# Optimization experiments

Hardware: AMD Instinct MI355X
Metric: run time of the kernel (lower is better)

The kernel has to match this reference:

```python
import math
import jax, jax.numpy as jnp
import numpy as np

B, S, H, BOT, RD, N, K = 4, 2048, 1024, 128, 48, 4096, 8

def setup_inputs() -> dict:
    key = jax.random.key(0)
    ks = jax.random.split(key, 12)
    hidden_states = jax.random.normal(ks[0], (B, S, H), jnp.float32)
    q_proj_w = jax.random.normal(ks[1], (BOT, H), jnp.float32) * (1.0 / math.sqrt(H))
    router_w = jax.random.normal(ks[2], (RD, BOT), jnp.float32) * (1.0 / math.sqrt(BOT))
    aux_keys = jax.random.normal(ks[3], (N, BOT), jnp.float32) * 0.01
    aux_values = jax.random.normal(ks[4], (N, H), jnp.float32) * 0.02
    # reliability per slot (log-domain additive mask derived from lifecycle state)
    reliability_mask = jax.random.uniform(ks[5], (N,), jnp.float32)
    unc_w1 = jax.random.normal(ks[6], (H // 4, H), jnp.float32) * (1.0 / math.sqrt(H))
    unc_b1 = jnp.zeros((H // 4,), jnp.float32)
    unc_w2 = jax.random.normal(ks[7], (1, H // 4), jnp.float32) * 0.02
    unc_b2 = jnp.zeros((1,), jnp.float32)
    gate_w1 = jnp.asarray(0.5, jnp.float32)
    gate_bias = jnp.asarray(-1.0, jnp.float32)
    return {"hidden_states": hidden_states, "q_proj_w": q_proj_w, "router_w": router_w,
            "aux_keys": aux_keys, "aux_values": aux_values, "reliability_mask": reliability_mask,
            "unc_w1": unc_w1, "unc_b1": unc_b1, "unc_w2": unc_w2, "unc_b2": unc_b2,
            "gate_w1": gate_w1, "gate_bias": gate_bias}

def reference(hidden_states, q_proj_w, router_w, aux_keys, aux_values, reliability_mask,
              unc_w1, unc_b1, unc_w2, unc_b2, gate_w1, gate_bias):
    # --- SlotRouter: project query/keys to router_dim, score, mask, top-k ---
    query = jnp.einsum('bsh,dh->bsd', hidden_states, q_proj_w)        # [B,S,BOT]
    rq = jnp.einsum('bsd,rd->bsr', query, router_w)                   # [B,S,RD]
    rk = jnp.einsum('nd,rd->nr', aux_keys, router_w)                  # [N,RD]
    scores = jnp.einsum('bsr,nr->bsn', rq, rk) / math.sqrt(RD)        # [B,S,N]
    scores = scores + reliability_mask[None, None, :]
    top_scores, top_idx = jax.lax.top_k(scores, K)                    # [B,S,K]
    # --- UncertaintyEstimator (HIDDEN_VARIANCE) ---
    mean = hidden_states.mean(axis=-1, keepdims=True)
    variance = ((hidden_states - mean) ** 2).mean(axis=-1)            # [B,S]
    log_var = jnp.log1p(variance)
    normalized_var = log_var / (log_var.mean() + 1e-6)
    h1 = jax.nn.gelu(jnp.einsum('bsh,fh->bsf', hidden_states, unc_w1) + unc_b1, approximate=False)
    learned = (jnp.einsum('bsf,of->bso', h1, unc_w2) + unc_b2)[..., 0]
    uncertainty = jnp.clip(normalized_var * 0.5 + jax.nn.sigmoid(learned) * 2.5, 0.0, 5.0)
    # --- Gate-1 scalar gate + slot aggregation ---
    gate = jax.nn.sigmoid(gate_w1 * uncertainty + gate_bias)          # [B,S]
    w = jax.nn.softmax(top_scores, axis=-1)                           # [B,S,K]
    v = aux_values[top_idx]                                           # [B,S,K,H]
    agg = jnp.einsum('bsk,bskh->bsh', w, v)
    out = hidden_states + gate[..., None] * agg
    return out
```

## Files before the change

### kernel.cpp

```cpp
#include <hip/hip_runtime.h>
#include <hip/hip_bf16.h>
#include <math.h>
#include <stdint.h>

#define NT 256
constexpr int Hc = 1024, BOTc = 128, RDc = 48, Nc = 4096;
constexpr int ROWS = 8192;
constexpr float INV_SQRT_RD = 0.14433756729740643f;

typedef short bf16x8 __attribute__((ext_vector_type(8)));
typedef float f32x4 __attribute__((ext_vector_type(4)));

__device__ __forceinline__ uint32_t umin32(uint32_t a, uint32_t b) { return a < b ? a : b; }
__device__ __forceinline__ uint32_t umax32(uint32_t a, uint32_t b) { return a > b ? a : b; }
__device__ __forceinline__ void ce_asc(uint32_t& x, uint32_t& y) {
  uint32_t lo = umin32(x, y), hi = umax32(x, y); x = lo; y = hi;
}
__device__ __forceinline__ uint32_t pack_score(float s, int slot) {
  uint32_t u = __float_as_uint(s);
  u = (u & 0x80000000u) ? ~u : (u | 0x80000000u);
  return (u & 0xFFFFF000u) | (uint32_t)slot;
}
__device__ __forceinline__ float unpack_score(uint32_t p) {
  uint32_t m = p & 0xFFFFF000u;
  uint32_t f = (m & 0x80000000u) ? (m ^ 0x80000000u) : ~m;
  return __uint_as_float(f);
}
__device__ __forceinline__ void merge_top8(uint32_t a[8], const uint32_t b[8]) {
  uint32_t m[8];
#pragma unroll
  for (int i = 0; i < 8; ++i) m[i] = umax32(a[i], b[7 - i]);
  ce_asc(m[0], m[4]); ce_asc(m[1], m[5]); ce_asc(m[2], m[6]); ce_asc(m[3], m[7]);
  ce_asc(m[0], m[2]); ce_asc(m[1], m[3]); ce_asc(m[4], m[6]); ce_asc(m[5], m[7]);
  ce_asc(m[0], m[1]); ce_asc(m[2], m[3]); ce_asc(m[4], m[5]); ce_asc(m[6], m[7]);
#pragma unroll
  for (int i = 0; i < 8; ++i) a[i] = m[i];
}
__device__ __forceinline__ void top8_insert(uint32_t top[8], uint32_t p) {
  if (p > top[0]) {
    top[0] = p;
    ce_asc(top[0], top[1]); ce_asc(top[1], top[2]); ce_asc(top[2], top[3]);
    ce_asc(top[3], top[4]); ce_asc(top[4], top[5]); ce_asc(top[5], top[6]);
    ce_asc(top[6], top[7]);
  }
}
__device__ __forceinline__ uint16_t bf16bits(float x) {
  uint32_t u = __float_as_uint(x);
  return (uint16_t)(((u + 0x7FFFu + ((u >> 16) & 1u)) >> 16) & 0xFFFFu);
}
__device__ __forceinline__ float bf2f(uint16_t h) {
  return __uint_as_float((uint32_t)h << 16);
}

constexpr int GP_W48 = 64, GP_RK = 768, GP_HB = 1024, GP_CVW = 32, GP_CVA = 512;
__global__ __launch_bounds__(256) void k_prep_all(
    const float* __restrict__ hidden, const float* __restrict__ q_proj_w,
    const float* __restrict__ router_w, const float* __restrict__ aux_keys,
    const float* __restrict__ aux_values, const float* __restrict__ rel,
    const float* __restrict__ unc_w1,
    uint16_t* __restrict__ xb, float* __restrict__ log_var,
    uint16_t* __restrict__ wcat, uint16_t* __restrict__ avb,
    uint16_t* __restrict__ rk_b) {
  int bid = blockIdx.x;
  int tid = threadIdx.x;
  if (bid < GP_W48) {
    __shared__ float rw[BOTc];
    int j = bid;
    if (j >= RDc) {
      for (int hh = tid; hh < Hc; hh += NT) wcat[(size_t)(256 + j) * Hc + hh] = 0;
      return;
    }
    for (int d = tid; d < BOTc; d += NT) rw[d] = router_w[j * BOTc + d];
    __syncthreads();
    float acc[4] = {0.f, 0.f, 0.f, 0.f};
#pragma unroll 4
    for (int d = 0; d < BOTc; ++d) {
      float r = rw[d];
#pragma unroll
      for (int jj = 0; jj < 4; ++jj)
        acc[jj] = fmaf(r, q_proj_w[d * Hc + tid + 256 * jj], acc[jj]);
    }
#pragma unroll
    for (int jj = 0; jj < 4; ++jj)
      wcat[(size_t)(256 + j) * Hc + tid + 256 * jj] = bf16bits(acc[jj]);
    return;
  }
  bid -= GP_W48;
  if (bid < GP_RK) {
    int gid = bid * NT + tid;
    int n = gid / RDc, r = gid - n * RDc;
    float acc = 0.f;
#pragma unroll 8
    for (int d = 0; d < BOTc; ++d)
      acc = fmaf(aux_keys[n * BOTc + d], router_w[r * BOTc + d], acc);
    rk_b[(size_t)n * 64 + r] = bf16bits(acc * INV_SQRT_RD);
    if (r < 16) rk_b[(size_t)n * 64 + 48 + r] = (r == 0) ? bf16bits(rel[n]) : (uint16_t)0;
    return;
  }
  bid -= GP_RK;
  if (bid < GP_HB) {
    int wave = tid >> 6, lane = tid & 63;
    int row = bid * 8 + wave * 2;
    const float4* r0 = reinterpret_cast<const float4*>(hidden + (size_t)row * Hc);
    const float4* r1 = reinterpret_cast<const float4*>(hidden + (size_t)(row + 1) * Hc);
    float4 v0[4], v1[4];
#pragma unroll
    for (int i = 0; i < 4; ++i) v0[i] = r0[lane + 64 * i];
#pragma unroll
    for (int i = 0; i < 4; ++i) v1[i] = r1[lane + 64 * i];
    float s0 = 0.f, q0 = 0.f, s1 = 0.f, q1 = 0.f;
#pragma unroll
    for (int i = 0; i < 4; ++i) {
      ushort4 h;
      h.x = bf16bits(v0[i].x); h.y = bf16bits(v0[i].y);
      h.z = bf16bits(v0[i].z); h.w = bf16bits(v0[i].w);
      *reinterpret_cast<ushort4*>(xb + (size_t)row * Hc + (lane + 64 * i) * 4) = h;
      s0 += v0[i].x + v0[i].y + v0[i].z + v0[i].w;
      q0 += v0[i].x * v0[i].x + v0[i].y * v0[i].y + v0[i].z * v0[i].z + v0[i].w * v0[i].w;
    }
#pragma unroll
    for (int i = 0; i < 4; ++i) {
      ushort4 h;
      h.x = bf16bits(v1[i].x); h.y = bf16bits(v1[i].y);
      h.z = bf16bits(v1[i].z); h.w = bf16bits(v1[i].w);
      *reinterpret_cast<ushort4*>(xb + (size_t)(row + 1) * Hc + (lane + 64 * i) * 4) = h;
      s1 += v1[i].x + v1[i].y + v1[i].z + v1[i].w;
      q1 += v1[i].x * v1[i].x + v1[i].y * v1[i].y + v1[i].z * v1[i].z + v1[i].w * v1[i].w;
    }
#pragma unroll
    for (int d = 32; d >= 1; d >>= 1) {
      s0 += __shfl_down(s0, d); q0 += __shfl_down(q0, d);
      s1 += __shfl_down(s1, d); q1 += __shfl_down(q1, d);
    }
    if (lane == 0) {
      float m0 = s0 * (1.f / Hc), m1 = s1 * (1.f / Hc);
      log_var[row]     = log1pf(q0 * (1.f / Hc) - m0 * m0);
      log_var[row + 1] = log1pf(q1 * (1.f / Hc) - m1 * m1);
    }
    return;
  }
  bid -= GP_HB;
  if (bid < GP_CVW) {
    float4 v[8];
    int base = bid * 2048 + tid;
#pragma unroll
    for (int i = 0; i < 8; ++i) v[i] = reinterpret_cast<const float4*>(unc_w1)[base + i * 256];
#pragma unroll
    for (int i = 0; i < 8; ++i) {
      ushort4 h;
      h.x = bf16bits(v[i].x); h.y = bf16bits(v[i].y);
      h.z = bf16bits(v[i].z); h.w = bf16bits(v[i].w);
      reinterpret_cast<ushort4*>(wcat)[base + i * 256] = h;
    }
    return;
  }
  bid -= GP_CVW;
  {
    float4 v[8];
    int base = bid * 2048 + tid;
#pragma unroll
    for (int i = 0; i < 8; ++i) v[i] = reinterpret_cast<const float4*>(aux_values)[base + i * 256];
#pragma unroll
    for (int i = 0; i < 8; ++i) {
      ushort4 h;
      h.x = bf16bits(v[i].x); h.y = bf16bits(v[i].y);
      h.z = bf16bits(v[i].z); h.w = bf16bits(v[i].w);
      reinterpret_cast<ushort4*>(avb)[base + i * 256] = h;
    }
  }
}

__global__ __launch_bounds__(256) void k_xw(const uint16_t* __restrict__ xb,
                                            const uint16_t* __restrict__ wcat,
                                            const float* __restrict__ b1,
                                            const float* __restrict__ w2,
                                            const float* __restrict__ log_var,
                                            float* __restrict__ stats,
                                            float* __restrict__ uncp,
                                            uint16_t* __restrict__ rq_b) {
  int bid = blockIdx.x;
  int tid = threadIdx.x;
  if (bid == 640) {
    float s = 0.f;
    for (int i = tid; i < ROWS; i += NT) s += log_var[i];
#pragma unroll
    for (int d = 32; d >= 1; d >>= 1) s += __shfl_down(s, d);
    __shared__ float ls[4];
    int lane = tid & 63, wv = tid >> 6;
    if (lane == 0) ls[wv] = s;
    __syncthreads();
    if (tid == 0) {
      s = ls[0] + ls[1] + ls[2] + ls[3];
      stats[0] = 1.f / (s * (1.f / ROWS) + 1e-6f);
    }
    return;
  }
  __shared__ uint16_t As[2][64 * 72];
  __shared__ uint16_t Bs[2][64 * 72];
  int wid = (bid & 7) * 80 + (bid >> 3);
  int rowg = wid / 5, colg = wid - rowg * 5;
  int wave = tid >> 6, lane = tid & 63;
  int l15 = lane & 15, lg = lane >> 4;
  int wr = wave >> 1, wc = wave & 1;
  int row0 = rowg * 64, n0 = colg * 64;
  int srow = tid >> 3, sseg = tid & 7;
  const uint16_t* agp = xb + (size_t)(row0 + srow) * Hc + sseg * 8;
  const uint16_t* bgp = wcat + (size_t)(n0 + srow) * Hc + sseg * 8;
  int sboff = srow * 72 + sseg * 8;
  int arow = wr * 32 + l15, brow = wc * 32 + l15;

  bf16x8 a0A = *reinterpret_cast<const bf16x8*>(agp);
  bf16x8 a1A = *reinterpret_cast<const bf16x8*>(agp + (size_t)32 * Hc);
  bf16x8 b0A = *reinterpret_cast<const bf16x8*>(bgp);
  bf16x8 b1A = *reinterpret_cast<const bf16x8*>(bgp + (size_t)32 * Hc);
  bf16x8 a0B = *reinterpret_cast<const bf16x8*>(agp + 64);
  bf16x8 a1B = *reinterpret_cast<const bf16x8*>(agp + (size_t)32 * Hc + 64);
  bf16x8 b0B = *reinterpret_cast<const bf16x8*>(bgp + 64);
  bf16x8 b1B = *reinterpret_cast<const bf16x8*>(bgp + (size_t)32 * Hc + 64);
  f32x4 acc00 = {0.f,0.f,0.f,0.f}, acc01 = {0.f,0.f,0.f,0.f};
  f32x4 acc10 = {0.f,0.f,0.f,0.f}, acc11 = {0.f,0.f,0.f,0.f};

  for (int tt = 0; tt < 16; tt += 2) {
    *reinterpret_cast<bf16x8*>(&As[0][sboff]) = a0A;
    *reinterpret_cast<bf16x8*>(&As[0][sboff + 32 * 72]) = a1A;
    *reinterpret_cast<bf16x8*>(&Bs[0][sboff]) = b0A;
    *reinterpret_cast<bf16x8*>(&Bs[0][sboff + 32 * 72]) = b1A;
    if (tt + 2 < 16) {
      int k0 = (tt + 2) * 64;
      a0A = *reinterpret_cast<const bf16x8*>(agp + k0);
      a1A = *reinterpret_cast<const bf16x8*>(agp + (size_t)32 * Hc + k0);
      b0A = *reinterpret_cast<const bf16x8*>(bgp + k0);
      b1A = *reinterpret_cast<const bf16x8*>(bgp + (size_t)32 * Hc + k0);
    }
    __syncthreads();
#pragma unroll
    for (int ks = 0; ks < 2; ++ks) {
      bf16x8 a0 = *reinterpret_cast<const bf16x8*>(&As[0][arow * 72 + ks * 32 + lg * 8]);
      bf16x8 a1 = *reinterpret_cast<const bf16x8*>(&As[0][(arow + 16) * 72 + ks * 32 + lg * 8]);
      bf16x8 b0 = *reinterpret_cast<const bf16x8*>(&Bs[0][brow * 72 + ks * 32 + lg * 8]);
      bf16x8 b1f = *reinterpret_cast<const bf16x8*>(&Bs[0][(brow + 16) * 72 + ks * 32 + lg * 8]);
      acc00 = __builtin_amdgcn_mfma_f32_16x16x32_bf16(a0, b0, acc00, 0, 0, 0);
      acc01 = __builtin_amdgcn_mfma_f32_16x16x32_bf16(a0, b1f, acc01, 0, 0, 0);
      acc10 = __builtin_amdgcn_mfma_f32_16x16x32_bf16(a1, b0, acc10, 0, 0, 0);
      acc11 = __builtin_amdgcn_mfma_f32_16x16x32_bf16(a1, b1f, acc11, 0, 0, 0);
    }
    *reinterpret_cast<bf16x8*>(&As[1][sboff]) = a0B;
    *reinterpret_cast<bf16x8*>(&As[1][sboff + 32 * 72]) = a1B;
    *reinterpret_cast<bf16x8*>(&Bs[1][sboff]) = b0B;
    *reinterpret_cast<bf16x8*>(&Bs[1][sboff + 32 * 72]) = b1B;
    if (tt + 3 < 16) {
      int k0 = (tt + 3) * 64;
      a0B = *reinterpret_cast<const bf16x8*>(agp + k0);
      a1B = *reinterpret_cast<const bf16x8*>(agp + (size_t)32 * Hc + k0);
      b0B = *reinterpret_cast<const bf16x8*>(bgp + k0);
      b1B = *reinterpret_cast<const bf16x8*>(bgp + (size_t)32 * Hc + k0);
    }
    __syncthreads();
#pragma unroll
    for (int ks = 0; ks < 2; ++ks) {
      bf16x8 a0 = *reinterpret_cast<const bf16x8*>(&As[1][arow * 72 + ks * 32 + lg * 8]);
      bf16x8 a1 = *reinterpret_cast<const bf16x8*>(&As[1][(arow + 16) * 72 + ks * 32 + lg * 8]);
      bf16x8 b0 = *reinterpret_cast<const bf16x8*>(&Bs[1][brow * 72 + ks * 32 + lg * 8]);
      bf16x8 b1f = *reinterpret_cast<const bf16x8*>(&Bs[1][(brow + 16) * 72 + ks * 32 + lg * 8]);
      acc00 = __builtin_amdgcn_mfma_f32_16x16x32_bf16(a0, b0, acc00, 0, 0, 0);
      acc01 = __builtin_amdgcn_mfma_f32_16x16x32_bf16(a0, b1f, acc01, 0, 0, 0);
      acc10 = __builtin_amdgcn_mfma_f32_16x16x32_bf16(a1, b0, acc10, 0, 0, 0);
      acc11 = __builtin_amdgcn_mfma_f32_16x16x32_bf16(a1, b1f, acc11, 0, 0, 0);
    }
  }
  if (colg < 4) {
    int gc0 = n0 + wc * 32 + l15;
    float b1v0 = b1[gc0],      w2v0 = w2[gc0];
    float b1v1 = b1[gc0 + 16], w2v1 = w2[gc0 + 16];
    int strip = colg * 2 + wc;
    float part0[4], part1[4];
#pragma unroll
    for (int r = 0; r < 4; ++r) {
      float x00 = acc00[r] + b1v0, x01 = acc01[r] + b1v1;
      float x10 = acc10[r] + b1v0, x11 = acc11[r] + b1v1;
      float g00 = 0.5f * x00 * (1.f + erff(x00 * 0.70710678118654752f));
      float g01 = 0.5f * x01 * (1.f + erff(x01 * 0.70710678118654752f));
      float g10 = 0.5f * x10 * (1.f + erff(x10 * 0.70710678118654752f));
      float g11 = 0.5f * x11 * (1.f + erff(x11 * 0.70710678118654752f));
      part0[r] = fmaf(g00, w2v0, g01 * w2v1);
      part1[r] = fmaf(g10, w2v0, g11 * w2v1);
    }
#pragma unroll
    for (int d = 1; d < 16; d <<= 1)
#pragma unroll
      for (int r = 0; r < 4; ++r) {
        part0[r] += __shfl_xor(part0[r], d);
        part1[r] += __shfl_xor(part1[r], d);
      }
    if (l15 == 0) {
#pragma unroll
      for (int r = 0; r < 4; ++r) {
        uncp[(size_t)(row0 + wr * 32 + lg * 4 + r) * 8 + strip] = part0[r];
        uncp[(size_t)(row0 + wr * 32 + 16 + lg * 4 + r) * 8 + strip] = part1[r];
      }
    }
  } else {
    int colA = wc * 32 + l15, colB = colA + 16;
#pragma unroll
    for (int r = 0; r < 4; ++r) {
      int rA = row0 + wr * 32 + lg * 4 + r, rB = rA + 16;
      uint16_t vA = bf16bits(acc00[r]);
      uint16_t vB = (colB == 48) ? (uint16_t)0x3F80u : bf16bits(acc01[r]);
      uint16_t uA = bf16bits(acc10[r]);
      uint16_t uB = (colB == 48) ? (uint16_t)0x3F80u : bf16bits(acc11[r]);
      rq_b[(size_t)rA * 64 + colA] = vA;
      rq_b[(size_t)rA * 64 + colB] = vB;
      rq_b[(size_t)rB * 64 + colA] = uA;
      rq_b[(size_t)rB * 64 + colB] = uB;
    }
  }
}

__global__ __launch_bounds__(256) void k_scores_mfma(const uint16_t* __restrict__ rq_b,
                                                     const uint16_t* __restrict__ rk_b,
                                                     uint32_t* __restrict__ cand) {
  int tid = threadIdx.x;
  int wave = tid >> 6, lane = tid & 63;
  int l15 = lane & 15, lg = lane >> 4;
  int rowg = blockIdx.x >> 3, range = blockIdx.x & 7;
  int q0 = rowg * 64 + wave * 16;
  const uint16_t* qp = rq_b + (size_t)(q0 + l15) * 64 + lg * 8;
  bf16x8 qf1 = *reinterpret_cast<const bf16x8*>(qp);
  bf16x8 qf2 = *reinterpret_cast<const bf16x8*>(qp + 32);
  uint32_t top[8];
#pragma unroll
  for (int q = 0; q < 8; ++q) top[q] = 0u;
  int sbase = range * 512;
  const uint16_t* kp = rk_b + (size_t)(sbase + l15) * 64 + lg * 8;
  bf16x8 a1c = *reinterpret_cast<const bf16x8*>(kp);
  bf16x8 a2c = *reinterpret_cast<const bf16x8*>(kp + 32);
  bf16x8 a3c = *reinterpret_cast<const bf16x8*>(kp + 1024);
  bf16x8 a4c = *reinterpret_cast<const bf16x8*>(kp + 1024 + 32);
#pragma unroll
  for (int t = 0; t < 32; t += 2) {
    bf16x8 a1n, a2n, a3n, a4n;
    if (t < 30) {
      const uint16_t* kpn = kp + (size_t)(t + 2) * 1024;
      a1n = *reinterpret_cast<const bf16x8*>(kpn);
      a2n = *reinterpret_cast<const bf16x8*>(kpn + 32);
      a3n = *reinterpret_cast<const bf16x8*>(kpn + 1024);
      a4n = *reinterpret_cast<const bf16x8*>(kpn + 1024 + 32);
    }
    int s0 = sbase + t * 16;
    f32x4 acc0 = {0.f,0.f,0.f,0.f}, acc1 = {0.f,0.f,0.f,0.f};
    acc0 = __builtin_amdgcn_mfma_f32_16x16x32_bf16(a1c, qf1, acc0, 0, 0, 0);
    acc1 = __builtin_amdgcn_mfma_f32_16x16x32_bf16(a3c, qf1, acc1, 0, 0, 0);
    acc0 = __builtin_amdgcn_mfma_f32_16x16x32_bf16(a2c, qf2, acc0, 0, 0, 0);
    acc1 = __builtin_amdgcn_mfma_f32_16x16x32_bf16(a4c, qf2, acc1, 0, 0, 0);
#pragma unroll
    for (int r = 0; r < 4; ++r) top8_insert(top, pack_score(acc0[r], s0 + lg * 4 + r));
#pragma unroll
    for (int r = 0; r < 4; ++r) top8_insert(top, pack_score(acc1[r], s0 + 16 + lg * 4 + r));
    if (t < 30) { a1c = a1n; a2c = a2n; a3c = a3n; a4c = a4n; }
  }
#pragma unroll
  for (int dd = 16; dd <= 32; dd <<= 1) {
    uint32_t o[8];
#pragma unroll
    for (int q = 0; q < 8; ++q) o[q] = __shfl_xor(top[q], dd);
    merge_top8(top, o);
  }
  if (lg == 0) {
    int row = q0 + l15;
#pragma unroll
    for (int q = 0; q < 8; ++q) cand[((size_t)row * 8 + range) * 8 + q] = top[q];
  }
}

__global__ __launch_bounds__(256) void k_final(const uint16_t* __restrict__ xb,
                                               const uint16_t* __restrict__ avb,
                                               const uint32_t* __restrict__ cand,
                                               const float* __restrict__ log_var,
                                               const float* __restrict__ uncp,
                                               const float* __restrict__ stats,
                                               const float* __restrict__ b2,
                                               const float* __restrict__ gw,
                                               const float* __restrict__ gb,
                                               float* __restrict__ out) {
  int tid = threadIdx.x;
  int wave = tid >> 6, lane = tid & 63;
  int row0 = blockIdx.x * 4;
  __shared__ float ws_[4][8]; __shared__ int wi_[4][8]; __shared__ float sg[4];
  {
    int row = row0 + wave;
    uint32_t l[8];
    float up = 0.f;
    if (lane < 8) {
      const uint32_t* c = cand + (size_t)row * 64 + lane * 8;
#pragma unroll
      for (int q = 0; q < 8; ++q) l[q] = c[q];
      up = uncp[(size_t)row * 8 + lane];
    } else {
#pragma unroll
      for (int q = 0; q < 8; ++q) l[q] = 0u;
    }
#pragma unroll
    for (int d = 1; d < 8; d <<= 1) {
      uint32_t o[8];
#pragma unroll
      for (int q = 0; q < 8; ++q) o[q] = __shfl_xor(l[q], d);
      merge_top8(l, o);
      up += __shfl_xor(up, d);
    }
    if (lane == 0) {
      float sc[8];
#pragma unroll
      for (int q = 0; q < 8; ++q) sc[q] = unpack_score(l[q]);
      float mx = sc[7];
      float e[8]; float sum = 0.f;
#pragma unroll
      for (int q = 0; q < 8; ++q) { e[q] = expf(sc[q] - mx); sum += e[q]; }
      float inv = 1.f / sum;
#pragma unroll
      for (int q = 0; q < 8; ++q) { ws_[wave][q] = e[q] * inv; wi_[wave][q] = (int)(l[q] & 0xFFFu); }
      float learned = up + b2[0];
      float nv = log_var[row] * stats[0];
      float sig = 1.f / (1.f + expf(-learned));
      float u = nv * 0.5f + sig * 2.5f;
      u = fminf(fmaxf(u, 0.f), 5.f);
      sg[wave] = 1.f / (1.f + expf(-(gw[0] * u + gb[0])));
    }
  }
  __syncthreads();
  int h0 = tid * 4;
#pragma unroll
  for (int rr = 0; rr < 4; ++rr) {
    int row = row0 + rr;
    ushort4 hb = *reinterpret_cast<const ushort4*>(xb + (size_t)row * Hc + h0);
    float ax = 0.f, ay = 0.f, az = 0.f, aw = 0.f;
#pragma unroll
    for (int k = 0; k < 8; ++k) {
      float w = ws_[rr][k];
      ushort4 v = *reinterpret_cast<const ushort4*>(avb + (size_t)wi_[rr][k] * Hc + h0);
      ax = fmaf(w, bf2f(v.x), ax); ay = fmaf(w, bf2f(v.y), ay);
      az = fmaf(w, bf2f(v.z), az); aw = fmaf(w, bf2f(v.w), aw);
    }
    float g = sg[rr];
    float4 o;
    o.x = bf2f(hb.x) + g * ax; o.y = bf2f(hb.y) + g * ay;
    o.z = bf2f(hb.z) + g * az; o.w = bf2f(hb.w) + g * aw;
    *reinterpret_cast<float4*>(out + (size_t)row * Hc + h0) = o;
  }
}

extern "C" void kernel_launch(void* const* d_in, const int* in_sizes, int n_in,
                              void* d_out, int out_size, void* d_ws, size_t ws_size,
                              hipStream_t stream) {
  const float* hidden     = (const float*)d_in[0];
  const float* q_proj_w   = (const float*)d_in[1];
  const float* router_w   = (const float*)d_in[2];
  const float* aux_keys   = (const float*)d_in[3];
  const float* aux_values = (const float*)d_in[4];
  const float* rel        = (const float*)d_in[5];
  const float* unc_w1     = (const float*)d_in[6];
  const float* unc_b1     = (const float*)d_in[7];
  const float* unc_w2     = (const float*)d_in[8];
  const float* unc_b2     = (const float*)d_in[9];
  const float* gate_w1    = (const float*)d_in[10];
  const float* gate_bias  = (const float*)d_in[11];
  float* out = (float*)d_out;

  uint8_t* w = (uint8_t*)d_ws;
  uint16_t* xb    = (uint16_t*)w;                 w += (size_t)ROWS * Hc * 2;
  uint16_t* wcat  = (uint16_t*)w;                 w += (size_t)320 * Hc * 2;
  uint16_t* avb   = (uint16_t*)w;                 w += (size_t)Nc * Hc * 2;
  uint16_t* rq_b  = (uint16_t*)w;                 w += (size_t)ROWS * 64 * 2;
  uint16_t* rk_b  = (uint16_t*)w;                 w += (size_t)Nc * 64 * 2;
  float* log_var  = (float*)w;                    w += (size_t)ROWS * 4;
  float* uncp     = (float*)w;                    w += (size_t)ROWS * 8 * 4;
  float* stats    = (float*)w;                    w += 256;
  uint32_t* cand  = (uint32_t*)w;                 w += (size_t)ROWS * 64 * 4;

  k_prep_all<<<GP_W48 + GP_RK + GP_HB + GP_CVW + GP_CVA, NT, 0, stream>>>(
      hidden, q_proj_w, router_w, aux_keys, aux_values, rel, unc_w1,
      xb, log_var, wcat, avb, rk_b);
  k_xw<<<641, NT, 0, stream>>>(xb, wcat, unc_b1, unc_w2, log_var, stats, uncp, rq_b);
  k_scores_mfma<<<1024, NT, 0, stream>>>(rq_b, rk_b, cand);
  k_final<<<ROWS / 4, NT, 0, stream>>>(xb, avb, cand, log_var, uncp,
                                       stats, unc_b2, gate_w1, gate_bias, out);
}
```

Measured before the change: 92.91 us.

## Fuse hidden-state bf16 conversion and variance into the GEMM A-tile loader

Drops the separate pass that converted hidden_states to a bf16 staging buffer and computed per-row variance. The GEMM kernel now loads fp32 hidden directly, converts to bf16 while staging into LDS, and the column-group-0 blocks accumulate sum and sum-of-squares for log_var. The log_var mean reduction moves into an extra block of the scores kernel, and the final kernel reads fp32 hidden instead of bf16. This saves a full write and read of the bf16 copy, in exchange for doubled A-tile global traffic in the GEMM (read five times across column groups) and extra conversion ALU work inside the GEMM loop.

```diff
diff --git a/kernel.cpp b/kernel.cpp
--- a/kernel.cpp
+++ b/kernel.cpp
@@ -51,14 +51,20 @@
 __device__ __forceinline__ float bf2f(uint16_t h) {
   return __uint_as_float((uint32_t)h << 16);
 }
-
-constexpr int GP_W48 = 64, GP_RK = 768, GP_HB = 1024, GP_CVW = 32, GP_CVA = 512;
+__device__ __forceinline__ bf16x8 cvt8(float4 a, float4 b) {
+  bf16x8 r;
+  r[0] = (short)bf16bits(a.x); r[1] = (short)bf16bits(a.y);
+  r[2] = (short)bf16bits(a.z); r[3] = (short)bf16bits(a.w);
+  r[4] = (short)bf16bits(b.x); r[5] = (short)bf16bits(b.y);
+  r[6] = (short)bf16bits(b.z); r[7] = (short)bf16bits(b.w);
+  return r;
+}
+
+constexpr int GP_W48 = 64, GP_RK = 768, GP_CVW = 32, GP_CVA = 512;
 __global__ __launch_bounds__(256) void k_prep_all(
-    const float* __restrict__ hidden, const float* __restrict__ q_proj_w,
-    const float* __restrict__ router_w, const float* __restrict__ aux_keys,
-    const float* __restrict__ aux_values, const float* __restrict__ rel,
-    const float* __restrict__ unc_w1,
-    uint16_t* __restrict__ xb, float* __restrict__ log_var,
+    const float* __restrict__ q_proj_w, const float* __restrict__ router_w,
+    const float* __restrict__ aux_keys, const float* __restrict__ aux_values,
+    const float* __restrict__ rel, const float* __restrict__ unc_w1,
     uint16_t* __restrict__ wcat, uint16_t* __restrict__ avb,
     uint16_t* __restrict__ rk_b) {
   int bid = blockIdx.x;
@@ -98,48 +104,6 @@
     return;
   }
   bid -= GP_RK;
-  if (bid < GP_HB) {
-    int wave = tid >> 6, lane = tid & 63;
-    int row = bid * 8 + wave * 2;
-    const float4* r0 = reinterpret_cast<const float4*>(hidden + (size_t)row * Hc);
-    const float4* r1 = reinterpret_cast<const float4*>(hidden + (size_t)(row + 1) * Hc);
-    float4 v0[4], v1[4];
-#pragma unroll
-    for (int i = 0; i < 4; ++i) v0[i] = r0[lane + 64 * i];
-#pragma unroll
-    for (int i = 0; i < 4; ++i) v1[i] = r1[lane + 64 * i];
-    float s0 = 0.f, q0 = 0.f, s1 = 0.f, q1 = 0.f;
-#pragma unroll
-    for (int i = 0; i < 4; ++i) {
-      ushort4 h;
-      h.x = bf16bits(v0[i].x); h.y = bf16bits(v0[i].y);
-      h.z = bf16bits(v0[i].z); h.w = bf16bits(v0[i].w);
-      *reinterpret_cast<ushort4*>(xb + (size_t)row * Hc + (lane + 64 * i) * 4) = h;
-      s0 += v0[i].x + v0[i].y + v0[i].z + v0[i].w;
-      q0 += v0[i].x * v0[i].x + v0[i].y * v0[i].y + v0[i].z * v0[i].z + v0[i].w * v0[i].w;
-    }
-#pragma unroll
-    for (int i = 0; i < 4; ++i) {
-      ushort4 h;
-      h.x = bf16bits(v1[i].x); h.y = bf16bits(v1[i].y);
-      h.z = bf16bits(v1[i].z); h.w = bf16bits(v1[i].w);
-      *reinterpret_cast<ushort4*>(xb + (size_t)(row + 1) * Hc + (lane + 64 * i) * 4) = h;
-      s1 += v1[i].x + v1[i].y + v1[i].z + v1[i].w;
-      q1 += v1[i].x * v1[i].x + v1[i].y * v1[i].y + v1[i].z * v1[i].z + v1[i].w * v1[i].w;
-    }
-#pragma unroll
-    for (int d = 32; d >= 1; d >>= 1) {
-      s0 += __shfl_down(s0, d); q0 += __shfl_down(q0, d);
-      s1 += __shfl_down(s1, d); q1 += __shfl_down(q1, d);
-    }
-    if (lane == 0) {
-      float m0 = s0 * (1.f / Hc), m1 = s1 * (1.f / Hc);
-      log_var[row]     = log1pf(q0 * (1.f / Hc) - m0 * m0);
-      log_var[row + 1] = log1pf(q1 * (1.f / Hc) - m1 * m1);
-    }
-    return;
-  }
-  bid -= GP_HB;
   if (bid < GP_CVW) {
     float4 v[8];
     int base = bid * 2048 + tid;
@@ -170,33 +134,17 @@
   }
 }
 
-__global__ __launch_bounds__(256) void k_xw(const uint16_t* __restrict__ xb,
+__global__ __launch_bounds__(256) void k_xw(const float* __restrict__ hidden,
                                             const uint16_t* __restrict__ wcat,
                                             const float* __restrict__ b1,
                                             const float* __restrict__ w2,
-                                            const float* __restrict__ log_var,
-                                            float* __restrict__ stats,
+                                            float* __restrict__ log_var,
                                             float* __restrict__ uncp,
                                             uint16_t* __restrict__ rq_b) {
+  __shared__ uint16_t As[2][64 * 72];
+  __shared__ uint16_t Bs[2][64 * 72];
   int bid = blockIdx.x;
   int tid = threadIdx.x;
-  if (bid == 640) {
-    float s = 0.f;
-    for (int i = tid; i < ROWS; i += NT) s += log_var[i];
-#pragma unroll
-    for (int d = 32; d >= 1; d >>= 1) s += __shfl_down(s, d);
-    __shared__ float ls[4];
-    int lane = tid & 63, wv = tid >> 6;
-    if (lane == 0) ls[wv] = s;
-    __syncthreads();
-    if (tid == 0) {
-      s = ls[0] + ls[1] + ls[2] + ls[3];
-      stats[0] = 1.f / (s * (1.f / ROWS) + 1e-6f);
-    }
-    return;
-  }
-  __shared__ uint16_t As[2][64 * 72];
-  __shared__ uint16_t Bs[2][64 * 72];
   int wid = (bid & 7) * 80 + (bid >> 3);
   int rowg = wid / 5, colg = wid - rowg * 5;
   int wave = tid >> 6, lane = tid & 63;
@@ -204,33 +152,50 @@
   int wr = wave >> 1, wc = wave & 1;
   int row0 = rowg * 64, n0 = colg * 64;
   int srow = tid >> 3, sseg = tid & 7;
-  const uint16_t* agp = xb + (size_t)(row0 + srow) * Hc + sseg * 8;
+  const float* agp0 = hidden + (size_t)(row0 + srow) * Hc + sseg * 8;
+  const float* agp1 = agp0 + (size_t)32 * Hc;
   const uint16_t* bgp = wcat + (size_t)(n0 + srow) * Hc + sseg * 8;
   int sboff = srow * 72 + sseg * 8;
   int arow = wr * 32 + l15, brow = wc * 32 + l15;
-
-  bf16x8 a0A = *reinterpret_cast<const bf16x8*>(agp);
-  bf16x8 a1A = *reinterpret_cast<const bf16x8*>(agp + (size_t)32 * Hc);
-  bf16x8 b0A = *reinterpret_cast<const bf16x8*>(bgp);
-  bf16x8 b1A = *reinterpret_cast<const bf16x8*>(bgp + (size_t)32 * Hc);
-  bf16x8 a0B = *reinterpret_cast<const bf16x8*>(agp + 64);
-  bf16x8 a1B = *reinterpret_cast<const bf16x8*>(agp + (size_t)32 * Hc + 64);
-  bf16x8 b0B = *reinterpret_cast<const bf16x8*>(bgp + 64);
-  bf16x8 b1B = *reinterpret_cast<const bf16x8*>(bgp + (size_t)32 * Hc + 64);
+  bool dovar = (colg == 0);
+  float vs0 = 0.f, vq0 = 0.f, vs1 = 0.f, vq1 = 0.f;
+
+  float4 xA0a = *reinterpret_cast<const float4*>(agp0);
+  float4 xA0b = *reinterpret_cast<const float4*>(agp0 + 4);
+  float4 xA1a = *reinterpret_cast<const float4*>(agp1);
+  float4 xA1b = *reinterpret_cast<const float4*>(agp1 + 4);
+  bf16x8 wA0 = *reinterpret_cast<const bf16x8*>(bgp);
+  bf16x8 wA1 = *reinterpret_cast<const bf16x8*>(bgp + (size_t)32 * Hc);
+  float4 xB0a = *reinterpret_cast<const float4*>(agp0 + 64);
+  float4 xB0b = *reinterpret_cast<const float4*>(agp0 + 68);
+  float4 xB1a = *reinterpret_cast<const float4*>(agp1 + 64);
+  float4 xB1b = *reinterpret_cast<const float4*>(agp1 + 68);
+  bf16x8 wB0 = *reinterpret_cast<const bf16x8*>(bgp + 64);
+  bf16x8 wB1 = *reinterpret_cast<const bf16x8*>(bgp + (size_t)32 * Hc + 64);
   f32x4 acc00 = {0.f,0.f,0.f,0.f}, acc01 = {0.f,0.f,0.f,0.f};
   f32x4 acc10 = {0.f,0.f,0.f,0.f}, acc11 = {0.f,0.f,0.f,0.f};
 
   for (int tt = 0; tt < 16; tt += 2) {
-    *reinterpret_cast<bf16x8*>(&As[0][sboff]) = a0A;
-    *reinterpret_cast<bf16x8*>(&As[0][sboff + 32 * 72]) = a1A;
-    *reinterpret_cast<bf16x8*>(&Bs[0][sboff]) = b0A;
-    *reinterpret_cast<bf16x8*>(&Bs[0][sboff + 32 * 72]) = b1A;
+    *reinterpret_cast<bf16x8*>(&As[0][sboff]) = cvt8(xA0a, xA0b);
+    *reinterpret_cast<bf16x8*>(&As[0][sboff + 32 * 72]) = cvt8(xA1a, xA1b);
+    *reinterpret_cast<bf16x8*>(&Bs[0][sboff]) = wA0;
+    *reinterpret_cast<bf16x8*>(&Bs[0][sboff + 32 * 72]) = wA1;
+    if (dovar) {
+      vs0 += xA0a.x + xA0a.y + xA0a.z + xA0a.w + xA0b.x + xA0b.y + xA0b.z + xA0b.w;
+      vq0 += xA0a.x*xA0a.x + xA0a.y*xA0a.y + xA0a.z*xA0a.z + xA0a.w*xA0a.w
+           + xA0b.x*xA0b.x + xA0b.y*xA0b.y + xA0b.z*xA0b.z + xA0b.w*xA0b.w;
+      vs1 += xA1a.x + xA1a.y + xA1a.z + xA1a.w + xA1b.x + xA1b.y + xA1b.z + xA1b.w;
+      vq1 += xA1a.x*xA1a.x + xA1a.y*xA1a.y + xA1a.z*xA1a.z + xA1a.w*xA1a.w
+           + xA1b.x*xA1b.x + xA1b.y*xA1b.y + xA1b.z*xA1b.z + xA1b.w*xA1b.w;
+    }
     if (tt + 2 < 16) {
       int k0 = (tt + 2) * 64;
-      a0A = *reinterpret_cast<const bf16x8*>(agp + k0);
-      a1A = *reinterpret_cast<const bf16x8*>(agp + (size_t)32 * Hc + k0);
-      b0A = *reinterpret_cast<const bf16x8*>(bgp + k0);
-      b1A = *reinterpret_cast<const bf16x8*>(bgp + (size_t)32 * Hc + k0);
+      xA0a = *reinterpret_cast<const float4*>(agp0 + k0);
+      xA0b = *reinterpret_cast<const float4*>(agp0 + k0 + 4);
+      xA1a = *reinterpret_cast<const float4*>(agp1 + k0);
+      xA1b = *reinterpret_cast<const float4*>(agp1 + k0 + 4);
+      wA0 = *reinterpret_cast<const bf16x8*>(bgp + k0);
+      wA1 = *reinterpret_cast<const bf16x8*>(bgp + (size_t)32 * Hc + k0);
     }
     __syncthreads();
 #pragma unroll
@@ -244,16 +209,26 @@
       acc10 = __builtin_amdgcn_mfma_f32_16x16x32_bf16(a1, b0, acc10, 0, 0, 0);
       acc11 = __builtin_amdgcn_mfma_f32_16x16x32_bf16(a1, b1f, acc11, 0, 0, 0);
     }
-    *reinterpret_cast<bf16x8*>(&As[1][sboff]) = a0B;
-    *reinterpret_cast<bf16x8*>(&As[1][sboff + 32 * 72]) = a1B;
-    *reinterpret_cast<bf16x8*>(&Bs[1][sboff]) = b0B;
-    *reinterpret_cast<bf16x8*>(&Bs[1][sboff + 32 * 72]) = b1B;
+    *reinterpret_cast<bf16x8*>(&As[1][sboff]) = cvt8(xB0a, xB0b);
+    *reinterpret_cast<bf16x8*>(&As[1][sboff + 32 * 72]) = cvt8(xB1a, xB1b);
+    *reinterpret_cast<bf16x8*>(&Bs[1][sboff]) = wB0;
+    *reinterpret_cast<bf16x8*>(&Bs[1][sboff + 32 * 72]) = wB1;
+    if (dovar) {
+      vs0 += xB0a.x + xB0a.y + xB0a.z + xB0a.w + xB0b.x + xB0b.y + xB0b.z + xB0b.w;
+      vq0 += xB0a.x*xB0a.x + xB0a.y*xB0a.y + xB0a.z*xB0a.z + xB0a.w*xB0a.w
+           + xB0b.x*xB0b.x + xB0b.y*xB0b.y + xB0b.z*xB0b.z + xB0b.w*xB0b.w;
+      vs1 += xB1a.x + xB1a.y + xB1a.z + xB1a.w + xB1b.x + xB1b.y + xB1b.z + xB1b.w;
+      vq1 += xB1a.x*xB1a.x + xB1a.y*xB1a.y + xB1a.z*xB1a.z + xB1a.w*xB1a.w
+           + xB1b.x*xB1b.x + xB1b.y*xB1b.y + xB1b.z*xB1b.z + xB1b.w*xB1b.w;
+    }
     if (tt + 3 < 16) {
       int k0 = (tt + 3) * 64;
-      a0B = *reinterpret_cast<const bf16x8*>(agp + k0);
-      a1B = *reinterpret_cast<const bf16x8*>(agp + (size_t)32 * Hc + k0);
-      b0B = *reinterpret_cast<const bf16x8*>(bgp + k0);
-      b1B = *reinterpret_cast<const bf16x8*>(bgp + (size_t)32 * Hc + k0);
+      xB0a = *reinterpret_cast<const float4*>(agp0 + k0);
+      xB0b = *reinterpret_cast<const float4*>(agp0 + k0 + 4);
+      xB1a = *reinterpret_cast<const float4*>(agp1 + k0);
+      xB1b = *reinterpret_cast<const float4*>(agp1 + k0 + 4);
+      wB0 = *reinterpret_cast<const bf16x8*>(bgp + k0);
+      wB1 = *reinterpret_cast<const bf16x8*>(bgp + (size_t)32 * Hc + k0);
     }
     __syncthreads();
 #pragma unroll
@@ -266,6 +241,18 @@
       acc01 = __builtin_amdgcn_mfma_f32_16x16x32_bf16(a0, b1f, acc01, 0, 0, 0);
       acc10 = __builtin_amdgcn_mfma_f32_16x16x32_bf16(a1, b0, acc10, 0, 0, 0);
       acc11 = __builtin_amdgcn_mfma_f32_16x16x32_bf16(a1, b1f, acc11, 0, 0, 0);
+    }
+  }
+  if (dovar) {
+#pragma unroll
+    for (int d = 4; d >= 1; d >>= 1) {
+      vs0 += __shfl_down(vs0, d); vq0 += __shfl_down(vq0, d);
+      vs1 += __shfl_down(vs1, d); vq1 += __shfl_down(vq1, d);
+    }
+    if ((lane & 7) == 0) {
+      float m0 = vs0 * (1.f / Hc), m1 = vs1 * (1.f / Hc);
+      log_var[row0 + srow]      = log1pf(vq0 * (1.f / Hc) - m0 * m0);
+      log_var[row0 + srow + 32] = log1pf(vq1 * (1.f / Hc) - m1 * m1);
     }
   }
   if (colg < 4) {
@@ -318,8 +305,25 @@
 
 __global__ __launch_bounds__(256) void k_scores_mfma(const uint16_t* __restrict__ rq_b,
                                                      const uint16_t* __restrict__ rk_b,
-                                                     uint32_t* __restrict__ cand) {
+                                                     uint32_t* __restrict__ cand,
+                                                     const float* __restrict__ log_var,
+                                                     float* __restrict__ stats) {
   int tid = threadIdx.x;
+  if (blockIdx.x == 1024) {
+    float s = 0.f;
+    for (int i = tid; i < ROWS; i += NT) s += log_var[i];
+#pragma unroll
+    for (int d = 32; d >= 1; d >>= 1) s += __shfl_down(s, d);
+    __shared__ float ls[4];
+    int lane = tid & 63, wv = tid >> 6;
+    if (lane == 0) ls[wv] = s;
+    __syncthreads();
+    if (tid == 0) {
+      s = ls[0] + ls[1] + ls[2] + ls[3];
+      stats[0] = 1.f / (s * (1.f / ROWS) + 1e-6f);
+    }
+    return;
+  }
   int wave = tid >> 6, lane = tid & 63;
   int l15 = lane & 15, lg = lane >> 4;
   int rowg = blockIdx.x >> 3, range = blockIdx.x & 7;
@@ -372,7 +376,7 @@
   }
 }
 
-__global__ __launch_bounds__(256) void k_final(const uint16_t* __restrict__ xb,
+__global__ __launch_bounds__(256) void k_final(const float* __restrict__ hidden,
                                                const uint16_t* __restrict__ avb,
                                                const uint32_t* __restrict__ cand,
                                                const float* __restrict__ log_var,
@@ -431,7 +435,7 @@
 #pragma unroll
   for (int rr = 0; rr < 4; ++rr) {
     int row = row0 + rr;
-    ushort4 hb = *reinterpret_cast<const ushort4*>(xb + (size_t)row * Hc + h0);
+    float4 hv = *reinterpret_cast<const float4*>(hidden + (size_t)row * Hc + h0);
     float ax = 0.f, ay = 0.f, az = 0.f, aw = 0.f;
 #pragma unroll
     for (int k = 0; k < 8; ++k) {
@@ -442,8 +446,8 @@
     }
     float g = sg[rr];
     float4 o;
-    o.x = bf2f(hb.x) + g * ax; o.y = bf2f(hb.y) + g * ay;
-    o.z = bf2f(hb.z) + g * az; o.w = bf2f(hb.w) + g * aw;
+    o.x = hv.x + g * ax; o.y = hv.y + g * ay;
+    o.z = hv.z + g * az; o.w = hv.w + g * aw;
     *reinterpret_cast<float4*>(out + (size_t)row * Hc + h0) = o;
   }
 }
@@ -466,7 +470,6 @@
   float* out = (float*)d_out;
 
   uint8_t* w = (uint8_t*)d_ws;
-  uint16_t* xb    = (uint16_t*)w;                 w += (size_t)ROWS * Hc * 2;
   uint16_t* wcat  = (uint16_t*)w;                 w += (size_t)320 * Hc * 2;
   uint16_t* avb   = (uint16_t*)w;                 w += (size_t)Nc * Hc * 2;
   uint16_t* rq_b  = (uint16_t*)w;                 w += (size_t)ROWS * 64 * 2;
@@ -476,11 +479,10 @@
   float* stats    = (float*)w;                    w += 256;
   uint32_t* cand  = (uint32_t*)w;                 w += (size_t)ROWS * 64 * 4;
 
-  k_prep_all<<<GP_W48 + GP_RK + GP_HB + GP_CVW + GP_CVA, NT, 0, stream>>>(
-      hidden, q_proj_w, router_w, aux_keys, aux_values, rel, unc_w1,
-      xb, log_var, wcat, avb, rk_b);
-  k_xw<<<641, NT, 0, stream>>>(xb, wcat, unc_b1, unc_w2, log_var, stats, uncp, rq_b);
-  k_scores_mfma<<<1024, NT, 0, stream>>>(rq_b, rk_b, cand);
-  k_final<<<ROWS / 4, NT, 0, stream>>>(xb, avb, cand, log_var, uncp,
+  k_prep_all<<<GP_W48 + GP_RK + GP_CVW + GP_CVA, NT, 0, stream>>>(
+      q_proj_w, router_w, aux_keys, aux_values, rel, unc_w1, wcat, avb, rk_b);
+  k_xw<<<640, NT, 0, stream>>>(hidden, wcat, unc_b1, unc_w2, log_var, uncp, rq_b);
+  k_scores_mfma<<<1025, NT, 0, stream>>>(rq_b, rk_b, cand, log_var, stats);
+  k_final<<<ROWS / 4, NT, 0, stream>>>(hidden, avb, cand, log_var, uncp,
                                        stats, unc_b2, gate_w1, gate_bias, out);
 }
```

Result: slower. 100.2 us (+7.8%).
